# Performance work log

Hardware: AMD Instinct MI355X
Metric: run time of the kernel (lower is better)

Reference implementation:

```python
import jax, jax.numpy as jnp
import numpy as np

B, N, T, D = 8, 2048, 512, 32


def _block(x1, x2, w, b):
    # Algebraically equivalent to Linear(cat([x1_i, x2_j])) without
    # materializing the (B, N1*N2, 2D) concat tensor:
    # score_ij = x1_i @ w[:D] + x2_j @ w[D:] + b
    d = x1.shape[-1]
    s1 = jnp.einsum('bnd,d->bn', x1, w[:d])  # (B, N1)
    s2 = jnp.einsum('bmd,d->bm', x2, w[d:])  # (B, N2)
    return s1[:, :, None] + s2[:, None, :] + b  # (B, N1, N2)


def setup_inputs() -> dict:
    key = jax.random.key(0)
    ks = jax.random.split(key, 10)
    inp = {
        'spatial_nodes': jax.random.normal(ks[0], (B, N, D), jnp.float32),
        'temporal_nodes': jax.random.normal(ks[1], (B, T, D), jnp.float32),
    }
    names = ['ss', 'tt', 'st', 'ts']
    for i, nm in enumerate(names):
        inp[f'w_{nm}'] = jax.random.normal(ks[2 + 2 * i], (2 * D,), jnp.float32) / np.sqrt(2 * D)
        inp[f'b_{nm}'] = jax.random.normal(ks[3 + 2 * i], (1,), jnp.float32) * 0.01
    return inp


def reference(spatial_nodes, temporal_nodes, w_ss, b_ss, w_tt, b_tt, w_st, b_st, w_ts, b_ts):
    ss = _block(spatial_nodes, spatial_nodes, w_ss, b_ss)    # (B, N, N)
    tt = _block(temporal_nodes, temporal_nodes, w_tt, b_tt)  # (B, T, T)
    st = _block(spatial_nodes, temporal_nodes, w_st, b_st)   # (B, N, T)
    ts = _block(temporal_nodes, spatial_nodes, w_ts, b_ts)   # (B, T, N)
    upper = jnp.concatenate([ss, st], axis=-1)  # (B, N, N+T)
    lower = jnp.concatenate([ts, tt], axis=-1)  # (B, T, N+T)
    _adj = jnp.concatenate([upper, lower], axis=-2)  # (B, N+T, N+T)
    adj = jnp.tanh(jax.nn.relu(_adj))
    return adj
```

## Files before the change

kernel.cpp:

```cpp
#include <hip/hip_runtime.h>

#define BB 8
#define NN 2048
#define TT 512
#define DD 32
#define SS (NN + TT)


__global__ __launch_bounds__(256) void precompute_scores(
    const float* __restrict__ sp,
    const float* __restrict__ tp,
    const float* __restrict__ w_ss, const float* __restrict__ b_ss,
    const float* __restrict__ w_tt, const float* __restrict__ b_tt,
    const float* __restrict__ w_st, const float* __restrict__ b_st,
    const float* __restrict__ w_ts, const float* __restrict__ b_ts,
    float* __restrict__ ws)
{
    int idx = blockIdx.x * blockDim.x + threadIdx.x;
    if (idx >= BB * SS) return;
    int b = idx / SS;
    int i = idx - b * SS;

    const float *v, *wl, *wr, *wcs, *wct;
    float bs, bt;
    if (i < NN) {
        v   = sp + ((size_t)b * NN + i) * DD;
        wl  = w_ss;       wr  = w_st;
        wcs = w_ss + DD;  wct = w_ts + DD;
        bs  = b_ss[0];    bt  = b_ts[0];
    } else {
        v   = tp + ((size_t)b * TT + (i - NN)) * DD;
        wl  = w_ts;       wr  = w_tt;
        wcs = w_st + DD;  wct = w_tt + DD;
        bs  = b_st[0];    bt  = b_tt[0];
    }

    float aL = 0.f, aR = 0.f, aS = 0.f, aT = 0.f;
#pragma unroll
    for (int d = 0; d < DD; ++d) {
        float x = v[d];
        aL = fmaf(x, wl[d],  aL);
        aR = fmaf(x, wr[d],  aR);
        aS = fmaf(x, wcs[d], aS);
        aT = fmaf(x, wct[d], aT);
    }

    float* rowL = ws;
    float* rowR = ws + 1 * BB * SS;
    float* colS = ws + 2 * BB * SS;
    float* colT = ws + 3 * BB * SS;
    rowL[idx] = aL;
    rowR[idx] = aR;
    colS[idx] = aS + bs;
    colT[idx] = aT + bt;
}

__device__ __forceinline__ float tanh_relu(float x) {
    float t = fmaxf(x, 0.f);
    float e = __expf(2.f * t);
    return fmaf(-2.f, __builtin_amdgcn_rcpf(e + 1.f), 1.f);
}

__global__ __launch_bounds__(640) void adj_kernel(
    const float* __restrict__ ws, float* __restrict__ out)
{
    int bid = blockIdx.x;
    int b = bid / SS;
    int r = bid - b * SS;

    const float* rowL = ws;
    const float* rowR = ws + 1 * BB * SS;
    const float* colS = ws + 2 * BB * SS;
    const float* colT = ws + 3 * BB * SS;

    float rL = rowL[bid];
    float rR = rowR[bid];
    const float* col = ((r < NN) ? colS : colT) + (size_t)b * SS;

    int c4 = threadIdx.x;
    float4 cv = ((const float4*)col)[c4];
    float rv = (c4 < NN / 4) ? rL : rR;

    float4 o;
    o.x = tanh_relu(rv + cv.x);
    o.y = tanh_relu(rv + cv.y);
    o.z = tanh_relu(rv + cv.z);
    o.w = tanh_relu(rv + cv.w);

    ((float4*)(out + (size_t)bid * SS))[c4] = o;
}

extern "C" void kernel_launch(void* const* d_in, const int* in_sizes, int n_in,
                              void* d_out, int out_size, void* d_ws, size_t ws_size,
                              hipStream_t stream) {
    const float* sp   = (const float*)d_in[0];
    const float* tp   = (const float*)d_in[1];
    const float* w_ss = (const float*)d_in[2];
    const float* b_ss = (const float*)d_in[3];
    const float* w_tt = (const float*)d_in[4];
    const float* b_tt = (const float*)d_in[5];
    const float* w_st = (const float*)d_in[6];
    const float* b_st = (const float*)d_in[7];
    const float* w_ts = (const float*)d_in[8];
    const float* b_ts = (const float*)d_in[9];
    float* out = (float*)d_out;
    float* ws  = (float*)d_ws;

    int nscore = BB * SS;
    precompute_scores<<<(nscore + 255) / 256, 256, 0, stream>>>(
        sp, tp, w_ss, b_ss, w_tt, b_tt, w_st, b_st, w_ts, b_ts, ws);

    adj_kernel<<<BB * SS, 640, 0, stream>>>(ws, out);
}
```

Measured before the change: 40.38 us.

## Fuse score precompute into adjacency kernel with 16-row blocks

Drops the separate score-precompute kernel and workspace round-trip. Each block now computes the column scores for its batch into shared memory, computes its 16 row scores, then writes 16 output rows, with each thread storing 8 contiguous floats per row. This removes one launch and the global workspace traffic. In exchange, every block recomputes all 2560 column dot products, so that redundant compute grows with the number of blocks.

```diff
diff --git a/kernel.cpp b/kernel.cpp
--- a/kernel.cpp
+++ b/kernel.cpp
@@ -5,55 +5,11 @@
 #define TT 512
 #define DD 32
 #define SS (NN + TT)
+#define RPB 16
+#define RGPB (SS / RPB)
+#define NTHR 320
 
-
-__global__ __launch_bounds__(256) void precompute_scores(
-    const float* __restrict__ sp,
-    const float* __restrict__ tp,
-    const float* __restrict__ w_ss, const float* __restrict__ b_ss,
-    const float* __restrict__ w_tt, const float* __restrict__ b_tt,
-    const float* __restrict__ w_st, const float* __restrict__ b_st,
-    const float* __restrict__ w_ts, const float* __restrict__ b_ts,
-    float* __restrict__ ws)
-{
-    int idx = blockIdx.x * blockDim.x + threadIdx.x;
-    if (idx >= BB * SS) return;
-    int b = idx / SS;
-    int i = idx - b * SS;
-
-    const float *v, *wl, *wr, *wcs, *wct;
-    float bs, bt;
-    if (i < NN) {
-        v   = sp + ((size_t)b * NN + i) * DD;
-        wl  = w_ss;       wr  = w_st;
-        wcs = w_ss + DD;  wct = w_ts + DD;
-        bs  = b_ss[0];    bt  = b_ts[0];
-    } else {
-        v   = tp + ((size_t)b * TT + (i - NN)) * DD;
-        wl  = w_ts;       wr  = w_tt;
-        wcs = w_st + DD;  wct = w_tt + DD;
-        bs  = b_st[0];    bt  = b_tt[0];
-    }
-
-    float aL = 0.f, aR = 0.f, aS = 0.f, aT = 0.f;
-#pragma unroll
-    for (int d = 0; d < DD; ++d) {
-        float x = v[d];
-        aL = fmaf(x, wl[d],  aL);
-        aR = fmaf(x, wr[d],  aR);
-        aS = fmaf(x, wcs[d], aS);
-        aT = fmaf(x, wct[d], aT);
-    }
-
-    float* rowL = ws;
-    float* rowR = ws + 1 * BB * SS;
-    float* colS = ws + 2 * BB * SS;
-    float* colT = ws + 3 * BB * SS;
-    rowL[idx] = aL;
-    rowR[idx] = aR;
-    colS[idx] = aS + bs;
-    colT[idx] = aT + bt;
-}
+typedef float vf4 __attribute__((ext_vector_type(4)));
 
 __device__ __forceinline__ float tanh_relu(float x) {
     float t = fmaxf(x, 0.f);
@@ -61,33 +17,81 @@
     return fmaf(-2.f, __builtin_amdgcn_rcpf(e + 1.f), 1.f);
 }
 
-__global__ __launch_bounds__(640) void adj_kernel(
-    const float* __restrict__ ws, float* __restrict__ out)
+__device__ __forceinline__ float dot32(const vf4* __restrict__ n4,
+                                       const vf4* __restrict__ w4) {
+    float acc = 0.f;
+#pragma unroll
+    for (int q = 0; q < DD / 4; ++q) {
+        vf4 x = n4[q], w = w4[q];
+        acc = fmaf(x.x, w.x, fmaf(x.y, w.y, fmaf(x.z, w.z, fmaf(x.w, w.w, acc))));
+    }
+    return acc;
+}
+
+__global__ __launch_bounds__(NTHR, 4) void adj_fused(
+    const float* __restrict__ sp,
+    const float* __restrict__ tp,
+    const float* __restrict__ w_ss, const float* __restrict__ b_ss,
+    const float* __restrict__ w_tt, const float* __restrict__ b_tt,
+    const float* __restrict__ w_st, const float* __restrict__ b_st,
+    const float* __restrict__ w_ts, const float* __restrict__ b_ts,
+    float* __restrict__ out)
 {
-    int bid = blockIdx.x;
-    int b = bid / SS;
-    int r = bid - b * SS;
+    __shared__ vf4 scol4[SS / 4];
+    __shared__ float srow[RPB][2];
 
-    const float* rowL = ws;
-    const float* rowR = ws + 1 * BB * SS;
-    const float* colS = ws + 2 * BB * SS;
-    const float* colT = ws + 3 * BB * SS;
+    int b  = blockIdx.x / RGPB;
+    int rg = blockIdx.x - b * RGPB;
+    int r0 = rg * RPB;
+    bool spatial = (r0 < NN);
 
-    float rL = rowL[bid];
-    float rR = rowR[bid];
-    const float* col = ((r < NN) ? colS : colT) + (size_t)b * SS;
+    int tid = threadIdx.x;
+    int c0  = tid * 8;
+    bool left = (c0 < NN);
 
-    int c4 = threadIdx.x;
-    float4 cv = ((const float4*)col)[c4];
-    float rv = (c4 < NN / 4) ? rL : rR;
+    const float* wc = (left ? (spatial ? w_ss : w_ts)
+                            : (spatial ? w_st : w_tt)) + DD;
+    float bc = left ? (spatial ? b_ss[0] : b_ts[0])
+                    : (spatial ? b_st[0] : b_tt[0]);
+    const float* nbase = left ? sp + ((size_t)b * NN + c0) * DD
+                              : tp + ((size_t)b * TT + (c0 - NN)) * DD;
+    const vf4* w4 = (const vf4*)wc;
 
-    float4 o;
-    o.x = tanh_relu(rv + cv.x);
-    o.y = tanh_relu(rv + cv.y);
-    o.z = tanh_relu(rv + cv.z);
-    o.w = tanh_relu(rv + cv.w);
+    float a[8];
+#pragma unroll
+    for (int k = 0; k < 8; ++k)
+        a[k] = dot32((const vf4*)(nbase + k * DD), w4) + bc;
+    scol4[2 * tid]     = (vf4){a[0], a[1], a[2], a[3]};
+    scol4[2 * tid + 1] = (vf4){a[4], a[5], a[6], a[7]};
 
-    ((float4*)(out + (size_t)bid * SS))[c4] = o;
+    if (tid < 2 * RPB) {
+        int rr = tid >> 1, side = tid & 1;
+        int r = r0 + rr;
+        const float* nv = spatial ? sp + ((size_t)b * NN + r) * DD
+                                  : tp + ((size_t)b * TT + (r - NN)) * DD;
+        const float* wr_ = (side == 0) ? (spatial ? w_ss : w_ts)
+                                       : (spatial ? w_st : w_tt);
+        srow[rr][side] = dot32((const vf4*)nv, (const vf4*)wr_);
+    }
+    __syncthreads();
+
+    vf4 cv0 = scol4[2 * tid];
+    vf4 cv1 = scol4[2 * tid + 1];
+    int side = left ? 0 : 1;
+    size_t rowbase = (size_t)(b * SS + r0) * SS;
+
+#pragma unroll 4
+    for (int r = 0; r < RPB; ++r) {
+        float rv = srow[r][side];
+        vf4 o0, o1;
+        o0.x = tanh_relu(rv + cv0.x); o0.y = tanh_relu(rv + cv0.y);
+        o0.z = tanh_relu(rv + cv0.z); o0.w = tanh_relu(rv + cv0.w);
+        o1.x = tanh_relu(rv + cv1.x); o1.y = tanh_relu(rv + cv1.y);
+        o1.z = tanh_relu(rv + cv1.z); o1.w = tanh_relu(rv + cv1.w);
+        vf4* p = (vf4*)(out + rowbase + (size_t)r * SS) + 2 * tid;
+        p[0] = o0;
+        p[1] = o1;
+    }
 }
 
 extern "C" void kernel_launch(void* const* d_in, const int* in_sizes, int n_in,
@@ -104,11 +108,7 @@
     const float* w_ts = (const float*)d_in[8];
     const float* b_ts = (const float*)d_in[9];
     float* out = (float*)d_out;
-    float* ws  = (float*)d_ws;
 
-    int nscore = BB * SS;
-    precompute_scores<<<(nscore + 255) / 256, 256, 0, stream>>>(
-        sp, tp, w_ss, b_ss, w_tt, b_tt, w_st, b_st, w_ts, b_ts, ws);
-
-    adj_kernel<<<BB * SS, 640, 0, stream>>>(ws, out);
+    adj_fused<<<BB * RGPB, NTHR, 0, stream>>>(
+        sp, tp, w_ss, b_ss, w_tt, b_tt, w_st, b_st, w_ts, b_ts, out);
 }
```

Measured after the change: 127.4 us. 215% more time.
